# Kernel optimization log

Hardware: AMD Instinct MI355X
Metric: run time of the kernel (lower is better)

The kernel has to match this reference:

```python
import jax, jax.numpy as jnp
import numpy as np

ENT = 500000
REL = 1000
D = 128
N = 65536


def setup_inputs() -> dict:
    key = jax.random.key(0)
    ks = jax.random.split(key, 9)
    pos_h = jax.random.randint(ks[0], (N,), 0, ENT)
    pos_t = jax.random.randint(ks[1], (N,), 0, ENT)
    pos_r = jax.random.randint(ks[2], (N,), 0, REL)
    neg_h = jax.random.randint(ks[3], (N,), 0, ENT)
    neg_t = jax.random.randint(ks[4], (N,), 0, ENT)
    neg_r = jax.random.randint(ks[5], (N,), 0, REL)
    # entity embeddings: xavier-init then L2-row-normalized
    ent = jax.random.normal(ks[6], (ENT, D), dtype=jnp.float32)
    ent = ent / jnp.linalg.norm(ent, axis=1, keepdims=True)
    # vvrel embeddings: plain randn (sized entity_total in the original)
    vvrel = jax.random.normal(ks[7], (ENT, D), dtype=jnp.float32)
    # relation bases: L2-row-normalized
    bases = jax.random.normal(ks[8], (REL, D), dtype=jnp.float32)
    bases = bases / jnp.linalg.norm(bases, axis=1, keepdims=True)
    return {"pos_h": pos_h, "pos_t": pos_t, "pos_r": pos_r,
            "neg_h": neg_h, "neg_t": neg_t, "neg_r": neg_r,
            "ent_emb": ent, "vvrel_emb": vvrel, "bases": bases}


def _hyperplane_project(x, v):
    # (I - v v^T / (v.v)) x, applied row-wise without materializing [N,d,d]
    coef = jnp.sum(v * x, axis=-1, keepdims=True) / jnp.sum(v * v, axis=-1, keepdims=True)
    return x - coef * v


def reference(pos_h, pos_t, pos_r, neg_h, neg_t, neg_r, ent_emb, vvrel_emb, bases):
    v_pos = bases[pos_r]  # [N, D]; original uses pos_r projection for BOTH pos and neg
    ph = _hyperplane_project(ent_emb[pos_h], v_pos)
    pt = _hyperplane_project(ent_emb[pos_t], v_pos)
    pr = _hyperplane_project(vvrel_emb[pos_r], v_pos)
    nh = _hyperplane_project(ent_emb[neg_h], v_pos)
    nt = _hyperplane_project(ent_emb[neg_t], v_pos)
    nr = _hyperplane_project(vvrel_emb[neg_r], v_pos)
    # L1_flag = True
    pos = jnp.sum(jnp.abs(ph + pr - pt), axis=1)
    neg = jnp.sum(jnp.abs(nh + nr - nt), axis=1)
    return (pos, neg)
```

## Files before the change

kernel.cpp:

```cpp
#include <hip/hip_runtime.h>

#define NSAMP 65536
#define DDIM  128

__global__ __launch_bounds__(256) void transh_kernel(
    const int* __restrict__ pos_h, const int* __restrict__ pos_t, const int* __restrict__ pos_r,
    const int* __restrict__ neg_h, const int* __restrict__ neg_t, const int* __restrict__ neg_r,
    const float* __restrict__ ent, const float* __restrict__ vvrel, const float* __restrict__ bases,
    float* __restrict__ out)
{
    const int tid  = blockIdx.x * blockDim.x + threadIdx.x;
    const int pair = tid >> 5;
    const int sub  = threadIdx.x & 31;
    const int s0   = pair << 1;
    if (s0 >= NSAMP) return;

    const int2 phI = *(const int2*)(pos_h + s0);
    const int2 ptI = *(const int2*)(pos_t + s0);
    const int2 prI = *(const int2*)(pos_r + s0);
    const int2 nhI = *(const int2*)(neg_h + s0);
    const int2 ntI = *(const int2*)(neg_t + s0);
    const int2 nrI = *(const int2*)(neg_r + s0);

    const float4 v0  = ((const float4*)(bases + (size_t)prI.x * DDIM))[sub];
    const float4 a0  = ((const float4*)(ent   + (size_t)phI.x * DDIM))[sub];
    const float4 c0  = ((const float4*)(ent   + (size_t)ptI.x * DDIM))[sub];
    const float4 b0  = ((const float4*)(vvrel + (size_t)prI.x * DDIM))[sub];
    const float4 na0 = ((const float4*)(ent   + (size_t)nhI.x * DDIM))[sub];
    const float4 nc0 = ((const float4*)(ent   + (size_t)ntI.x * DDIM))[sub];
    const float4 nb0 = ((const float4*)(vvrel + (size_t)nrI.x * DDIM))[sub];
    const float4 v1  = ((const float4*)(bases + (size_t)prI.y * DDIM))[sub];
    const float4 a1  = ((const float4*)(ent   + (size_t)phI.y * DDIM))[sub];
    const float4 c1  = ((const float4*)(ent   + (size_t)ptI.y * DDIM))[sub];
    const float4 b1  = ((const float4*)(vvrel + (size_t)prI.y * DDIM))[sub];
    const float4 na1 = ((const float4*)(ent   + (size_t)nhI.y * DDIM))[sub];
    const float4 nc1 = ((const float4*)(ent   + (size_t)ntI.y * DDIM))[sub];
    const float4 nb1 = ((const float4*)(vvrel + (size_t)nrI.y * DDIM))[sub];

    float4 sp0, sn0;
    sp0.x = a0.x + b0.x - c0.x;   sp0.y = a0.y + b0.y - c0.y;
    sp0.z = a0.z + b0.z - c0.z;   sp0.w = a0.w + b0.w - c0.w;
    sn0.x = na0.x + nb0.x - nc0.x; sn0.y = na0.y + nb0.y - nc0.y;
    sn0.z = na0.z + nb0.z - nc0.z; sn0.w = na0.w + nb0.w - nc0.w;

    float vv0  = v0.x * v0.x + v0.y * v0.y + v0.z * v0.z + v0.w * v0.w;
    float vsp0 = v0.x * sp0.x + v0.y * sp0.y + v0.z * sp0.z + v0.w * sp0.w;
    float vsn0 = v0.x * sn0.x + v0.y * sn0.y + v0.z * sn0.z + v0.w * sn0.w;

    float4 sp1, sn1;
    sp1.x = a1.x + b1.x - c1.x;   sp1.y = a1.y + b1.y - c1.y;
    sp1.z = a1.z + b1.z - c1.z;   sp1.w = a1.w + b1.w - c1.w;
    sn1.x = na1.x + nb1.x - nc1.x; sn1.y = na1.y + nb1.y - nc1.y;
    sn1.z = na1.z + nb1.z - nc1.z; sn1.w = na1.w + nb1.w - nc1.w;

    float vv1  = v1.x * v1.x + v1.y * v1.y + v1.z * v1.z + v1.w * v1.w;
    float vsp1 = v1.x * sp1.x + v1.y * sp1.y + v1.z * sp1.z + v1.w * sp1.w;
    float vsn1 = v1.x * sn1.x + v1.y * sn1.y + v1.z * sn1.z + v1.w * sn1.w;

    #pragma unroll
    for (int off = 16; off > 0; off >>= 1) {
        vv0  += __shfl_xor(vv0,  off, 64);
        vsp0 += __shfl_xor(vsp0, off, 64);
        vsn0 += __shfl_xor(vsn0, off, 64);
        vv1  += __shfl_xor(vv1,  off, 64);
        vsp1 += __shfl_xor(vsp1, off, 64);
        vsn1 += __shfl_xor(vsn1, off, 64);
    }

    const float cp0 = vsp0 / vv0;
    const float cn0 = vsn0 / vv0;
    const float cp1 = vsp1 / vv1;
    const float cn1 = vsn1 / vv1;

    float ap0 = fabsf(sp0.x - cp0 * v0.x) + fabsf(sp0.y - cp0 * v0.y)
              + fabsf(sp0.z - cp0 * v0.z) + fabsf(sp0.w - cp0 * v0.w);
    float an0 = fabsf(sn0.x - cn0 * v0.x) + fabsf(sn0.y - cn0 * v0.y)
              + fabsf(sn0.z - cn0 * v0.z) + fabsf(sn0.w - cn0 * v0.w);
    float ap1 = fabsf(sp1.x - cp1 * v1.x) + fabsf(sp1.y - cp1 * v1.y)
              + fabsf(sp1.z - cp1 * v1.z) + fabsf(sp1.w - cp1 * v1.w);
    float an1 = fabsf(sn1.x - cn1 * v1.x) + fabsf(sn1.y - cn1 * v1.y)
              + fabsf(sn1.z - cn1 * v1.z) + fabsf(sn1.w - cn1 * v1.w);

    #pragma unroll
    for (int off = 16; off > 0; off >>= 1) {
        ap0 += __shfl_xor(ap0, off, 64);
        an0 += __shfl_xor(an0, off, 64);
        ap1 += __shfl_xor(ap1, off, 64);
        an1 += __shfl_xor(an1, off, 64);
    }

    if (sub == 0) {
        *(float2*)(out + s0)         = make_float2(ap0, ap1);
        *(float2*)(out + NSAMP + s0) = make_float2(an0, an1);
    }
}

extern "C" void kernel_launch(void* const* d_in, const int* in_sizes, int n_in,
                              void* d_out, int out_size, void* d_ws, size_t ws_size,
                              hipStream_t stream) {
    const int*   pos_h = (const int*)d_in[0];
    const int*   pos_t = (const int*)d_in[1];
    const int*   pos_r = (const int*)d_in[2];
    const int*   neg_h = (const int*)d_in[3];
    const int*   neg_t = (const int*)d_in[4];
    const int*   neg_r = (const int*)d_in[5];
    const float* ent   = (const float*)d_in[6];
    const float* vvrel = (const float*)d_in[7];
    const float* bases = (const float*)d_in[8];
    float* out = (float*)d_out;

    const int threads = 256;
    const int blocks  = (NSAMP / 2 * 32) / threads;
    transh_kernel<<<blocks, threads, 0, stream>>>(
        pos_h, pos_t, pos_r, neg_h, neg_t, neg_r, ent, vvrel, bases, out);
}
```

Measured before the change: 420.8 us.

## Stride half-waves over samples with prefetched indices instead of pairing samples

The grid is cut to 16384 half-waves, each handling 4 samples strided across the batch in a loop, instead of each half-wave handling two adjacent samples. Indices for the next iteration are prefetched before the current gather is used, so index load latency overlaps with gather latency. The cost is fewer bytes in flight per half-wave, since one sample's seven rows are loaded per iteration rather than two samples' fourteen, plus loop serialization and less occupancy headroom.

```diff
diff --git a/kernel.cpp b/kernel.cpp
--- a/kernel.cpp
+++ b/kernel.cpp
@@ -1,7 +1,9 @@
 #include <hip/hip_runtime.h>
 
-#define NSAMP 65536
-#define DDIM  128
+#define NSAMP  65536
+#define DDIM   128
+#define HWAVES 16384
+#define ITERS  (NSAMP / HWAVES)
 
 __global__ __launch_bounds__(256) void transh_kernel(
     const int* __restrict__ pos_h, const int* __restrict__ pos_t, const int* __restrict__ pos_r,
@@ -9,89 +11,73 @@
     const float* __restrict__ ent, const float* __restrict__ vvrel, const float* __restrict__ bases,
     float* __restrict__ out)
 {
-    const int tid  = blockIdx.x * blockDim.x + threadIdx.x;
-    const int pair = tid >> 5;
-    const int sub  = threadIdx.x & 31;
-    const int s0   = pair << 1;
-    if (s0 >= NSAMP) return;
+    const int hw  = (blockIdx.x * blockDim.x + threadIdx.x) >> 5;
+    const int sub = threadIdx.x & 31;
 
-    const int2 phI = *(const int2*)(pos_h + s0);
-    const int2 ptI = *(const int2*)(pos_t + s0);
-    const int2 prI = *(const int2*)(pos_r + s0);
-    const int2 nhI = *(const int2*)(neg_h + s0);
-    const int2 ntI = *(const int2*)(neg_t + s0);
-    const int2 nrI = *(const int2*)(neg_r + s0);
-
-    const float4 v0  = ((const float4*)(bases + (size_t)prI.x * DDIM))[sub];
-    const float4 a0  = ((const float4*)(ent   + (size_t)phI.x * DDIM))[sub];
-    const float4 c0  = ((const float4*)(ent   + (size_t)ptI.x * DDIM))[sub];
-    const float4 b0  = ((const float4*)(vvrel + (size_t)prI.x * DDIM))[sub];
-    const float4 na0 = ((const float4*)(ent   + (size_t)nhI.x * DDIM))[sub];
-    const float4 nc0 = ((const float4*)(ent   + (size_t)ntI.x * DDIM))[sub];
-    const float4 nb0 = ((const float4*)(vvrel + (size_t)nrI.x * DDIM))[sub];
-    const float4 v1  = ((const float4*)(bases + (size_t)prI.y * DDIM))[sub];
-    const float4 a1  = ((const float4*)(ent   + (size_t)phI.y * DDIM))[sub];
-    const float4 c1  = ((const float4*)(ent   + (size_t)ptI.y * DDIM))[sub];
-    const float4 b1  = ((const float4*)(vvrel + (size_t)prI.y * DDIM))[sub];
-    const float4 na1 = ((const float4*)(ent   + (size_t)nhI.y * DDIM))[sub];
-    const float4 nc1 = ((const float4*)(ent   + (size_t)ntI.y * DDIM))[sub];
-    const float4 nb1 = ((const float4*)(vvrel + (size_t)nrI.y * DDIM))[sub];
-
-    float4 sp0, sn0;
-    sp0.x = a0.x + b0.x - c0.x;   sp0.y = a0.y + b0.y - c0.y;
-    sp0.z = a0.z + b0.z - c0.z;   sp0.w = a0.w + b0.w - c0.w;
-    sn0.x = na0.x + nb0.x - nc0.x; sn0.y = na0.y + nb0.y - nc0.y;
-    sn0.z = na0.z + nb0.z - nc0.z; sn0.w = na0.w + nb0.w - nc0.w;
-
-    float vv0  = v0.x * v0.x + v0.y * v0.y + v0.z * v0.z + v0.w * v0.w;
-    float vsp0 = v0.x * sp0.x + v0.y * sp0.y + v0.z * sp0.z + v0.w * sp0.w;
-    float vsn0 = v0.x * sn0.x + v0.y * sn0.y + v0.z * sn0.z + v0.w * sn0.w;
-
-    float4 sp1, sn1;
-    sp1.x = a1.x + b1.x - c1.x;   sp1.y = a1.y + b1.y - c1.y;
-    sp1.z = a1.z + b1.z - c1.z;   sp1.w = a1.w + b1.w - c1.w;
-    sn1.x = na1.x + nb1.x - nc1.x; sn1.y = na1.y + nb1.y - nc1.y;
-    sn1.z = na1.z + nb1.z - nc1.z; sn1.w = na1.w + nb1.w - nc1.w;
-
-    float vv1  = v1.x * v1.x + v1.y * v1.y + v1.z * v1.z + v1.w * v1.w;
-    float vsp1 = v1.x * sp1.x + v1.y * sp1.y + v1.z * sp1.z + v1.w * sp1.w;
-    float vsn1 = v1.x * sn1.x + v1.y * sn1.y + v1.z * sn1.z + v1.w * sn1.w;
+    int ph_i = pos_h[hw];
+    int pt_i = pos_t[hw];
+    int pr_i = pos_r[hw];
+    int nh_i = neg_h[hw];
+    int nt_i = neg_t[hw];
+    int nr_i = neg_r[hw];
 
     #pragma unroll
-    for (int off = 16; off > 0; off >>= 1) {
-        vv0  += __shfl_xor(vv0,  off, 64);
-        vsp0 += __shfl_xor(vsp0, off, 64);
-        vsn0 += __shfl_xor(vsn0, off, 64);
-        vv1  += __shfl_xor(vv1,  off, 64);
-        vsp1 += __shfl_xor(vsp1, off, 64);
-        vsn1 += __shfl_xor(vsn1, off, 64);
-    }
+    for (int k = 0; k < ITERS; ++k) {
+        const int s = hw + k * HWAVES;
 
-    const float cp0 = vsp0 / vv0;
-    const float cn0 = vsn0 / vv0;
-    const float cp1 = vsp1 / vv1;
-    const float cn1 = vsn1 / vv1;
+        const float4 a  = ((const float4*)(ent   + (size_t)ph_i * DDIM))[sub];
+        const float4 c  = ((const float4*)(ent   + (size_t)pt_i * DDIM))[sub];
+        const float4 na = ((const float4*)(ent   + (size_t)nh_i * DDIM))[sub];
+        const float4 nc = ((const float4*)(ent   + (size_t)nt_i * DDIM))[sub];
+        const float4 v  = ((const float4*)(bases + (size_t)pr_i * DDIM))[sub];
+        const float4 b  = ((const float4*)(vvrel + (size_t)pr_i * DDIM))[sub];
+        const float4 nb = ((const float4*)(vvrel + (size_t)nr_i * DDIM))[sub];
 
-    float ap0 = fabsf(sp0.x - cp0 * v0.x) + fabsf(sp0.y - cp0 * v0.y)
-              + fabsf(sp0.z - cp0 * v0.z) + fabsf(sp0.w - cp0 * v0.w);
-    float an0 = fabsf(sn0.x - cn0 * v0.x) + fabsf(sn0.y - cn0 * v0.y)
-              + fabsf(sn0.z - cn0 * v0.z) + fabsf(sn0.w - cn0 * v0.w);
-    float ap1 = fabsf(sp1.x - cp1 * v1.x) + fabsf(sp1.y - cp1 * v1.y)
-              + fabsf(sp1.z - cp1 * v1.z) + fabsf(sp1.w - cp1 * v1.w);
-    float an1 = fabsf(sn1.x - cn1 * v1.x) + fabsf(sn1.y - cn1 * v1.y)
-              + fabsf(sn1.z - cn1 * v1.z) + fabsf(sn1.w - cn1 * v1.w);
+        if (k + 1 < ITERS) {
+            const int s2 = s + HWAVES;
+            ph_i = pos_h[s2];
+            pt_i = pos_t[s2];
+            pr_i = pos_r[s2];
+            nh_i = neg_h[s2];
+            nt_i = neg_t[s2];
+            nr_i = neg_r[s2];
+        }
 
-    #pragma unroll
-    for (int off = 16; off > 0; off >>= 1) {
-        ap0 += __shfl_xor(ap0, off, 64);
-        an0 += __shfl_xor(an0, off, 64);
-        ap1 += __shfl_xor(ap1, off, 64);
-        an1 += __shfl_xor(an1, off, 64);
-    }
+        float4 sp, sn;
+        sp.x = a.x + b.x - c.x;     sp.y = a.y + b.y - c.y;
+        sp.z = a.z + b.z - c.z;     sp.w = a.w + b.w - c.w;
+        sn.x = na.x + nb.x - nc.x;  sn.y = na.y + nb.y - nc.y;
+        sn.z = na.z + nb.z - nc.z;  sn.w = na.w + nb.w - nc.w;
 
-    if (sub == 0) {
-        *(float2*)(out + s0)         = make_float2(ap0, ap1);
-        *(float2*)(out + NSAMP + s0) = make_float2(an0, an1);
+        float vv  = v.x * v.x  + v.y * v.y  + v.z * v.z  + v.w * v.w;
+        float vsp = v.x * sp.x + v.y * sp.y + v.z * sp.z + v.w * sp.w;
+        float vsn = v.x * sn.x + v.y * sn.y + v.z * sn.z + v.w * sn.w;
+
+        #pragma unroll
+        for (int off = 16; off > 0; off >>= 1) {
+            vv  += __shfl_xor(vv,  off, 64);
+            vsp += __shfl_xor(vsp, off, 64);
+            vsn += __shfl_xor(vsn, off, 64);
+        }
+
+        const float cp = vsp / vv;
+        const float cn = vsn / vv;
+
+        float ap = fabsf(sp.x - cp * v.x) + fabsf(sp.y - cp * v.y)
+                 + fabsf(sp.z - cp * v.z) + fabsf(sp.w - cp * v.w);
+        float an = fabsf(sn.x - cn * v.x) + fabsf(sn.y - cn * v.y)
+                 + fabsf(sn.z - cn * v.z) + fabsf(sn.w - cn * v.w);
+
+        #pragma unroll
+        for (int off = 16; off > 0; off >>= 1) {
+            ap += __shfl_xor(ap, off, 64);
+            an += __shfl_xor(an, off, 64);
+        }
+
+        if (sub == 0) {
+            out[s]         = ap;
+            out[NSAMP + s] = an;
+        }
     }
 }
 
@@ -110,7 +96,7 @@
     float* out = (float*)d_out;
 
     const int threads = 256;
-    const int blocks  = (NSAMP / 2 * 32) / threads;
+    const int blocks  = (HWAVES * 32) / threads;
     transh_kernel<<<blocks, threads, 0, stream>>>(
         pos_h, pos_t, pos_r, neg_h, neg_t, neg_r, ent, vvrel, bases, out);
 }
```

New measurement: 422.9 us. Within noise of the previous version (+0.5%).
